# Kernel optimization log

Measured on AMD Instinct MI355X. Metric: run time of the kernel, lower is better.

Reference implementation:

```python
import jax, jax.numpy as jnp
import numpy as np
from jax import lax

WS = 7          # window size
SHIFT = 3       # shift size
HEADS = 16
DIM = 512
NREF = 100
H_IMG = 112
W_IMG = 112
BATCH = 2
HD = DIM // HEADS
SCALE = HD ** (-0.5)
EPS = 1e-5


def _layernorm(x, w, b):
    mu = jnp.mean(x, axis=-1, keepdims=True)
    var = jnp.mean((x - mu) ** 2, axis=-1, keepdims=True)
    return (x - mu) / jnp.sqrt(var + EPS) * w + b


def _rel_pos_index():
    coords = np.stack(np.meshgrid(np.arange(WS), np.arange(WS), indexing='ij'))  # (2,ws,ws)
    cf = coords.reshape(2, -1)
    rel = cf[:, :, None] - cf[:, None, :]
    rel = rel.transpose(1, 2, 0).astype(np.int64)
    rel[..., 0] += WS - 1
    rel[..., 1] += WS - 1
    rel[..., 0] *= 2 * WS - 1
    return rel.sum(-1).reshape(-1)  # (N*N,)

_RPI = _rel_pos_index()


def setup_inputs() -> dict:
    key = jax.random.key(0)
    ks = jax.random.split(key, 16)
    C = DIM
    s = 0.02
    x = jax.random.normal(ks[0], (BATCH, H_IMG * W_IMG, C), jnp.float32)
    x_ref = jax.random.normal(ks[1], (BATCH, NREF, C), jnp.float32)
    # shifted-window attention mask (standard Swin construction)
    img = np.zeros((H_IMG, W_IMG))
    cnt = 0
    for hs in (slice(0, -WS), slice(-WS, -SHIFT), slice(-SHIFT, None)):
        for ws_ in (slice(0, -WS), slice(-WS, -SHIFT), slice(-SHIFT, None)):
            img[hs, ws_] = cnt
            cnt += 1
    mw = img.reshape(H_IMG // WS, WS, W_IMG // WS, WS).transpose(0, 2, 1, 3).reshape(-1, WS * WS)
    am = mw[:, None, :] - mw[:, :, None]
    mask = jnp.asarray(np.where(am != 0, -100.0, 0.0), jnp.float32)  # (nW, N, N)
    return dict(
        x=x, x_ref=x_ref, mask=mask,
        norm1_w=jnp.ones((C,), jnp.float32), norm1_b=jnp.zeros((C,), jnp.float32),
        qkv_w=jax.random.normal(ks[2], (3 * C, C), jnp.float32) * s,
        qkv_b=jnp.zeros((3 * C,), jnp.float32),
        diff_mu=jax.random.normal(ks[3], (1, 1, C), jnp.float32),
        diff_logsigma=jax.random.normal(ks[4], (1, 1, C), jnp.float32) * s,
        rpb_table=jax.random.normal(ks[5], ((2 * WS - 1) ** 2, HEADS), jnp.float32) * s,
        ref_qk_w=jax.random.normal(ks[6], (2 * C, C), jnp.float32) * s,
        ref_qk_b=jnp.zeros((2 * C,), jnp.float32),
        conv_w=jax.random.normal(ks[7], (HEADS, HEADS, 3, 3), jnp.float32) * s,
        conv_b=jnp.zeros((HEADS,), jnp.float32),
        proj_w=jax.random.normal(ks[8], (C, C), jnp.float32) * s,
        proj_b=jnp.zeros((C,), jnp.float32),
        norm2_w=jnp.ones((C,), jnp.float32), norm2_b=jnp.zeros((C,), jnp.float32),
        fc1_w=jax.random.normal(ks[9], (4 * C, C), jnp.float32) * s,
        fc1_b=jnp.zeros((4 * C,), jnp.float32),
        fc2_w=jax.random.normal(ks[10], (C, 4 * C), jnp.float32) * s,
        fc2_b=jnp.zeros((C,), jnp.float32),
        Hh=H_IMG, Ww=W_IMG,
    )


def _window_attention(xw, mask, x_ref, qkv_w, qkv_b, diff_mu, diff_logsigma,
                      rpb_table, ref_qk_w, ref_qk_b, conv_w, conv_b, proj_w, proj_b):
    B_, N, C = xw.shape
    rB = x_ref.shape[0]
    n_win = B_ // rB
    qkv = (xw @ qkv_w.T + qkv_b).reshape(B_, N, 3, HEADS, HD).transpose(2, 0, 3, 1, 4)
    q, k, v = qkv[0], qkv[1], qkv[2]  # (B_, heads, N, hd)
    # reference tokens -> q/v with reparameterized shift/scale
    ref_qk = (x_ref @ ref_qk_w.T + ref_qk_b).reshape(rB, NREF, 2, C).transpose(2, 0, 1, 3)
    ref_q = diff_mu + jnp.exp(diff_logsigma) * ref_qk[0]
    ref_q = ref_q.reshape(rB, NREF, HEADS, HD).transpose(0, 2, 1, 3)
    ref_v = ref_qk[1].reshape(rB, NREF, HEADS, HD).transpose(0, 2, 1, 3)
    ref_k = jnp.repeat(ref_q, n_win, axis=0)  # (B_, heads, nref, hd)
    ref_v = jnp.repeat(ref_v, n_win, axis=0)
    ra = jnp.einsum('bhnd,bhrd->bhnr', q, ref_k)  # (B_, heads, N, nref)
    ra = ra.reshape(rB, n_win, HEADS, N, NREF).transpose(0, 2, 1, 3, 4).reshape(rB, HEADS, n_win * N, NREF)
    # 3 rounds of conv diffusion + layernorm(no affine) + gelu, residual
    for _ in range(3):
        u = lax.conv_general_dilated(ra, conv_w, (1, 1), 'SAME',
                                     dimension_numbers=('NCHW', 'OIHW', 'NCHW'))
        u = u + conv_b[None, :, None, None]
        mu = jnp.mean(u, axis=(-2, -1), keepdims=True)
        var = jnp.mean((u - mu) ** 2, axis=(-2, -1), keepdims=True)
        u = jax.nn.gelu((u - mu) / jnp.sqrt(var + EPS), approximate=False)
        ra = ra + u
    ra = ra.reshape(rB, HEADS, n_win, N, NREF).transpose(0, 2, 1, 3, 4).reshape(B_, HEADS, N, NREF)
    ra = jax.nn.softmax(ra, axis=-1)
    q_new = jnp.einsum('bhnr,bhrd->bhnd', ra, ref_v) * SCALE
    attn = jnp.einsum('bhnd,bhmd->bhnm', q_new, k)
    rpb = rpb_table[_RPI].reshape(N, N, HEADS).transpose(2, 0, 1)  # (heads, N, N)
    attn = attn + rpb[None]
    nW = mask.shape[0]
    attn = attn.reshape(B_ // nW, nW, HEADS, N, N) + mask[None, :, None]
    attn = jax.nn.softmax(attn.reshape(B_, HEADS, N, N), axis=-1)
    out = jnp.einsum('bhnm,bhmd->bhnd', attn, v).transpose(0, 2, 1, 3).reshape(B_, N, C)
    return out @ proj_w.T + proj_b


def reference(x, x_ref, mask, norm1_w, norm1_b, qkv_w, qkv_b, diff_mu, diff_logsigma,
              rpb_table, ref_qk_w, ref_qk_b, conv_w, conv_b, proj_w, proj_b,
              norm2_w, norm2_b, fc1_w, fc1_b, fc2_w, fc2_b, Hh, Ww):
    B, L, C = x.shape
    shortcut = x
    xn = _layernorm(x, norm1_w, norm1_b).reshape(B, Hh, Ww, C)
    # cyclic shift
    sx = jnp.roll(xn, (-SHIFT, -SHIFT), axis=(1, 2))
    # window partition -> (B*nWin, ws*ws, C)
    xw = sx.reshape(B, Hh // WS, WS, Ww // WS, WS, C).transpose(0, 1, 3, 2, 4, 5).reshape(-1, WS * WS, C)
    aw = _window_attention(xw, mask, x_ref, qkv_w, qkv_b, diff_mu, diff_logsigma,
                           rpb_table, ref_qk_w, ref_qk_b, conv_w, conv_b, proj_w, proj_b)
    # window reverse
    sx = aw.reshape(B, Hh // WS, Ww // WS, WS, WS, C).transpose(0, 1, 3, 2, 4, 5).reshape(B, Hh, Ww, C)
    xn = jnp.roll(sx, (SHIFT, SHIFT), axis=(1, 2)).reshape(B, L, C)
    x = shortcut + xn
    h = _layernorm(x, norm2_w, norm2_b)
    h = jax.nn.gelu(h @ fc1_w.T + fc1_b, approximate=False)
    return x + (h @ fc2_w.T + fc2_b)
```

## Files before the change

### kernel.cpp

```cpp
#include <hip/hip_runtime.h>
#include <hip/hip_bf16.h>

typedef __attribute__((ext_vector_type(8))) short short8;
typedef __attribute__((ext_vector_type(8))) unsigned short ushort8;
typedef __attribute__((ext_vector_type(4))) float f32x4;
typedef __attribute__((ext_vector_type(4))) unsigned int u32x4;
typedef __attribute__((ext_vector_type(2))) unsigned int u32x2;

#define DEV __device__ __forceinline__

DEV float gelu_f(float x) { return 0.5f * x * (1.f + erff(x * 0.70710678118654752440f)); }

DEV float bf2f(unsigned short s) {
  unsigned int t = ((unsigned int)s) << 16;
  float f; __builtin_memcpy(&f, &t, 4); return f;
}
DEV unsigned short f2bf(float f) {
  __hip_bfloat16 b = __float2bfloat16(f);
  unsigned short s; __builtin_memcpy(&s, &b, 2); return s;
}

DEV void async_copy16(void* lds, const void* g) {
  __builtin_amdgcn_global_load_lds(
      (const __attribute__((address_space(1))) unsigned int*)g,
      (__attribute__((address_space(3))) unsigned int*)lds, 16, 0, 0);
}

DEV void block_reduce2(float& s, float& s2) {
  __shared__ float red[8];
  int tid = threadIdx.x;
#pragma unroll
  for (int o = 32; o > 0; o >>= 1) { s += __shfl_down(s, o); s2 += __shfl_down(s2, o); }
  if ((tid & 63) == 0) { red[tid >> 6] = s; red[4 + (tid >> 6)] = s2; }
  __syncthreads();
  s  = red[0] + red[1] + red[2] + red[3];
  s2 = red[4] + red[5] + red[6] + red[7];
}

__global__ __launch_bounds__(256) void f2b_kernel(const float* __restrict__ in,
                                                  __hip_bfloat16* __restrict__ o, int n) {
  int i = blockIdx.x * 256 + threadIdx.x;
  if (i < n) o[i] = __float2bfloat16(in[i]);
}

__global__ __launch_bounds__(256) void maskb_kernel(const float* __restrict__ mask,
                                                    unsigned short* __restrict__ maskB) {
  int i = blockIdx.x * 256 + threadIdx.x;
  int m = i % 56, rest = i / 56;
  int n = rest % 49, win = rest / 49;
  unsigned short v = 0;
  if (m < 49) v = f2bf(mask[((size_t)win * 49 + n) * 49 + m]);
  maskB[i] = v;
}

__global__ __launch_bounds__(256) void rpbt_kernel(const float* __restrict__ rpb,
                                                   unsigned short* __restrict__ rpbT) {
  int i = blockIdx.x * 256 + threadIdx.x;
  if (i >= 43904) return;
  int m = i % 56, rest = i / 56;
  int n = rest % 49, h = rest / 49;
  unsigned short v = 0;
  if (m < 49) {
    int rp = (n / 7 - m / 7 + 6) * 13 + (n % 7 - m % 7 + 6);
    v = f2bf(rpb[rp * 16 + h]);
  }
  rpbT[i] = v;
}

__global__ __launch_bounds__(256) void ln1_window_kernel(
    const float* __restrict__ x, const float* __restrict__ w, const float* __restrict__ b,
    __hip_bfloat16* __restrict__ xw) {
  int tid = threadIdx.x;
  int wave = tid >> 6, lane = tid & 63;
  int t = blockIdx.x * 4 + wave;
  int b_ = t / 49, n = t % 49;
  int bb = b_ >> 8, win = b_ & 255;
  int wi = win >> 4, wj = win & 15;
  int ii = n / 7, jj = n % 7;
  int sh = (wi * 7 + ii + 3) % 112;
  int sw = (wj * 7 + jj + 3) % 112;
  const float* row = x + ((size_t)bb * 12544 + sh * 112 + sw) * 512;
  f32x4 v0 = *reinterpret_cast<const f32x4*>(&row[lane * 8]);
  f32x4 v1 = *reinterpret_cast<const f32x4*>(&row[lane * 8 + 4]);
  float s = 0.f, s2 = 0.f;
#pragma unroll
  for (int j = 0; j < 4; j++) {
    s += v0[j] + v1[j];
    s2 += v0[j] * v0[j] + v1[j] * v1[j];
  }
#pragma unroll
  for (int o = 1; o < 64; o <<= 1) { s += __shfl_xor(s, o); s2 += __shfl_xor(s2, o); }
  float mu = s * (1.f / 512.f);
  float rstd = rsqrtf(s2 * (1.f / 512.f) - mu * mu + 1e-5f);
  f32x4 w0 = *reinterpret_cast<const f32x4*>(&w[lane * 8]);
  f32x4 w1 = *reinterpret_cast<const f32x4*>(&w[lane * 8 + 4]);
  f32x4 c0 = *reinterpret_cast<const f32x4*>(&b[lane * 8]);
  f32x4 c1 = *reinterpret_cast<const f32x4*>(&b[lane * 8 + 4]);
  ushort8 o8;
#pragma unroll
  for (int j = 0; j < 4; j++) {
    o8[j]     = f2bf((v0[j] - mu) * rstd * w0[j] + c0[j]);
    o8[4 + j] = f2bf((v1[j] - mu) * rstd * w1[j] + c1[j]);
  }
  *reinterpret_cast<ushort8*>((unsigned short*)xw + (size_t)t * 512 + lane * 8) = o8;
}

template <int EPI>
__global__ __launch_bounds__(256) void gemm_bt(
    const __hip_bfloat16* __restrict__ A, const __hip_bfloat16* __restrict__ B,
    const float* __restrict__ bias, float* __restrict__ outF,
    __hip_bfloat16* __restrict__ outB, int M, int N, int K) {
  __shared__ __align__(16) __hip_bfloat16 As[128 * 64];
  __shared__ __align__(16) __hip_bfloat16 Bs[128 * 64];
  int m0 = blockIdx.x * 128, n0 = blockIdx.y * 128;
  int tid = threadIdx.x;
  int wave = tid >> 6, lane = tid & 63;
  int wm = (wave & 1) * 64, wn = (wave >> 1) * 64;
  int lrow = lane & 15, kq = lane >> 4;
  int srow = lane >> 3, scol = (lane & 7) * 8;
  f32x4 acc[4][4] = {};
  for (int k0 = 0; k0 < K; k0 += 64) {
    int rb = wave * 32;
#pragma unroll
    for (int i = 0; i < 4; i++) {
      int row = rb + i * 8 + srow;
      async_copy16(&As[(rb + i * 8) * 64], &A[(size_t)(m0 + row) * K + k0 + scol]);
      async_copy16(&Bs[(rb + i * 8) * 64], &B[(size_t)(n0 + row) * K + k0 + scol]);
    }
    __syncthreads();
#pragma unroll
    for (int ks = 0; ks < 2; ks++) {
      short8 af[4], bf[4];
#pragma unroll
      for (int t = 0; t < 4; t++) {
        af[t] = *reinterpret_cast<const short8*>(&As[(wm + t * 16 + lrow) * 64 + ks * 32 + kq * 8]);
        bf[t] = *reinterpret_cast<const short8*>(&Bs[(wn + t * 16 + lrow) * 64 + ks * 32 + kq * 8]);
      }
#pragma unroll
      for (int tm = 0; tm < 4; tm++)
#pragma unroll
        for (int tn = 0; tn < 4; tn++)
          acc[tm][tn] = __builtin_amdgcn_mfma_f32_16x16x32_bf16(af[tm], bf[tn], acc[tm][tn], 0, 0, 0);
    }
    __syncthreads();
  }
#pragma unroll
  for (int tm = 0; tm < 4; tm++) {
#pragma unroll
    for (int tn = 0; tn < 4; tn++) {
      int col = n0 + wn + tn * 16 + lrow;
      float bv = bias[col];
#pragma unroll
      for (int r = 0; r < 4; r++) {
        int row = m0 + wm + tm * 16 + kq * 4 + r;
        float v = acc[tm][tn][r] + bv;
        size_t o = (size_t)row * N + col;
        if (EPI == 1) outB[o] = __float2bfloat16(v);
        else if (EPI == 2) outB[o] = __float2bfloat16(gelu_f(v));
        else outF[o] += v;
      }
    }
  }
}

__global__ __launch_bounds__(256) void ref_kernel(
    const float* __restrict__ x_ref, const float* __restrict__ w, const float* __restrict__ bias,
    const float* __restrict__ diff_mu, const float* __restrict__ diff_ls,
    unsigned short* __restrict__ refq, unsigned short* __restrict__ refvT) {
  int blk = blockIdx.x;
  int b = blk / 100, r = blk % 100;
  __shared__ float xs[512];
  int tid = threadIdx.x;
  const float* xr = x_ref + (size_t)(b * 100 + r) * 512;
  xs[tid] = xr[tid];
  xs[tid + 256] = xr[tid + 256];
  __syncthreads();
#pragma unroll
  for (int cc = 0; cc < 4; cc++) {
    int c = cc * 256 + tid;
    const float* wr = w + (size_t)c * 512;
    float s = bias[c];
    for (int k = 0; k < 512; k++) s += xs[k] * wr[k];
    if (c < 512) {
      float v = diff_mu[c] + expf(diff_ls[c]) * s;
      int hh = c >> 5, d = c & 31;
      refq[((size_t)(b * 16 + hh) * 100 + r) * 32 + d] = f2bf(v);
    } else {
      int c2 = c - 512, hh = c2 >> 5, d = c2 & 31;
      refvT[(((size_t)b * 16 + hh) * 32 + d) * 100 + r] = f2bf(s);
    }
  }
}

__global__ __launch_bounds__(256) void ra_kernel(
    const __hip_bfloat16* __restrict__ q, const unsigned short* __restrict__ refq,
    __hip_bfloat16* __restrict__ ra) {
  __shared__ __align__(16) unsigned short q_s[64 * 40];
  __shared__ __align__(16) unsigned short rq_s[112 * 40];
  int blk = blockIdx.x;
  int b_ = blk >> 4, h = blk & 15;
  int rb = b_ >> 8, win = b_ & 255;
  int tid = threadIdx.x;
  int wave = tid >> 6, lane = tid & 63;
  int lrow = lane & 15, kq = lane >> 4;
  u32x4 z4 = {};
  const unsigned short* qb = (const unsigned short*)q + (size_t)b_ * 49 * 512 + h * 32;
  for (int i = tid; i < 196; i += 256) {
    int n = i >> 2, c = i & 3;
    *reinterpret_cast<u32x4*>(&q_s[n * 40 + c * 8]) =
        *reinterpret_cast<const u32x4*>(&qb[n * 512 + c * 8]);
  }
  for (int i = tid; i < 60; i += 256) {
    int n = 49 + (i >> 2), c = i & 3;
    *reinterpret_cast<u32x4*>(&q_s[n * 40 + c * 8]) = z4;
  }
  const unsigned short* rqg = refq + (size_t)(rb * 16 + h) * 3200;
  for (int i = tid; i < 400; i += 256) {
    int r = i >> 2, c = i & 3;
    *reinterpret_cast<u32x4*>(&rq_s[r * 40 + c * 8]) =
        *reinterpret_cast<const u32x4*>(&rqg[r * 32 + c * 8]);
  }
  for (int i = tid; i < 48; i += 256) {
    int r = 100 + (i >> 2), c = i & 3;
    *reinterpret_cast<u32x4*>(&rq_s[r * 40 + c * 8]) = z4;
  }
  __syncthreads();
  short8 a = *reinterpret_cast<const short8*>(&q_s[(wave * 16 + lrow) * 40 + kq * 8]);
  unsigned short* ra_base = (unsigned short*)ra + ((size_t)(rb * 16 + h) * 12544 + win * 49) * 100;
  f32x4 zero = {};
#pragma unroll
  for (int nt = 0; nt < 7; nt++) {
    short8 b = *reinterpret_cast<const short8*>(&rq_s[(nt * 16 + lrow) * 40 + kq * 8]);
    f32x4 c = __builtin_amdgcn_mfma_f32_16x16x32_bf16(a, b, zero, 0, 0, 0);
    int col = nt * 16 + lrow;
#pragma unroll
    for (int r = 0; r < 4; r++) {
      int n = wave * 16 + kq * 4 + r;
      if (n < 49 && col < 100) ra_base[n * 100 + col] = f2bf(c[r]);
    }
  }
}

__global__ __launch_bounds__(256) void conv_kernel(
    const __hip_bfloat16* __restrict__ ra_, const float* __restrict__ cw, const float* __restrict__ cb,
    __hip_bfloat16* __restrict__ u_, float* __restrict__ psum, float* __restrict__ psumsq) {
  __shared__ __align__(16) unsigned short in_s[6 * 103 * 24];
  __shared__ __align__(16) unsigned short w_s[16 * 160];
  __shared__ float sred_s[4][16], sred_s2[4][16];
  const unsigned short* ra = (const unsigned short*)ra_;
  unsigned short* u = (unsigned short*)u_;
  int yt = blockIdx.x, bb = blockIdx.y;
  int y0 = yt * 4;
  int tid = threadIdx.x;
  int wave = tid >> 6, lane = tid & 63;
  int lrow = lane & 15, kq = lane >> 4;
  for (int i = tid; i < 2560; i += 256) {
    int co = i / 160, k = i % 160;
    unsigned short v = 0;
    if (k < 144) {
      int ci = k & 15, p = k >> 4;
      v = f2bf(cw[(co * 16 + ci) * 9 + p]);
    }
    w_s[i] = v;
  }
  for (int i = tid; i < 288; i += 256) {
    int ci = i & 15, rem = i >> 4;
    int yl = rem / 3, xs = rem % 3;
    int xl = (xs == 0) ? 0 : (100 + xs);
    in_s[(yl * 103 + xl) * 24 + ci] = 0;
  }
  if (tid < 192) {
    int unit = tid >> 1, par = tid & 1;
    int ci = unit / 6, yl = unit % 6;
    int gy = y0 - 1 + yl;
    bool rv = (gy >= 0 && gy < 12544);
    const unsigned short* rp = ra + (((size_t)bb * 16 + ci) * 12544 + (rv ? gy : 0)) * 100;
    unsigned short* lp = &in_s[(yl * 103 + 1) * 24 + ci];
#pragma unroll 4
    for (int c = par; c < 25; c += 2) {
      u32x2 d = {0u, 0u};
      if (rv) d = *reinterpret_cast<const u32x2*>(&rp[c * 4]);
      lp[(c * 4 + 0) * 24] = (unsigned short)(d[0] & 0xffff);
      lp[(c * 4 + 1) * 24] = (unsigned short)(d[0] >> 16);
      lp[(c * 4 + 2) * 24] = (unsigned short)(d[1] & 0xffff);
      lp[(c * 4 + 3) * 24] = (unsigned short)(d[1] >> 16);
    }
  }
  __syncthreads();

  short8 afr[5];
#pragma unroll
  for (int c = 0; c < 5; c++)
    afr[c] = *reinterpret_cast<const short8*>(&w_s[lrow * 160 + c * 32 + kq * 8]);
  int kqh = kq >> 1, ci0 = (kq & 1) * 8;
  int kyA[5], kxA[5];
#pragma unroll
  for (int c = 0; c < 5; c++) {
    int p = c * 2 + kqh; if (p > 8) p = 0;
    kyA[c] = p / 3; kxA[c] = p % 3;
  }
  float bias_r[4];
#pragma unroll
  for (int r = 0; r < 4; r++) bias_r[r] = cb[kq * 4 + r];
  float s_r[4] = {0.f, 0.f, 0.f, 0.f}, s2_r[4] = {0.f, 0.f, 0.f, 0.f};

  int yl = wave;
  int gy = y0 + yl;
#pragma unroll
  for (int xg = 0; xg < 7; xg++) {
    int px = xg * 16 + lrow;
    int pxc = px < 100 ? px : 99;
    f32x4 acc = {};
#pragma unroll
    for (int c = 0; c < 5; c++) {
      short8 bfrag = *reinterpret_cast<const short8*>(
          &in_s[((yl + kyA[c]) * 103 + pxc + kxA[c]) * 24 + ci0]);
      acc = __builtin_amdgcn_mfma_f32_16x16x32_bf16(afr[c], bfrag, acc, 0, 0, 0);
    }
    bool valid = px < 100;
#pragma unroll
    for (int r = 0; r < 4; r++) {
      float v = acc[r] + bias_r[r];
      if (valid) {
        u[(((size_t)bb * 16 + kq * 4 + r) * 12544 + gy) * 100 + px] = f2bf(v);
        s_r[r] += v; s2_r[r] += v * v;
      }
    }
  }
#pragma unroll
  for (int o = 1; o < 16; o <<= 1)
#pragma unroll
    for (int r = 0; r < 4; r++) { s_r[r] += __shfl_xor(s_r[r], o); s2_r[r] += __shfl_xor(s2_r[r], o); }
  if (lrow == 0)
#pragma unroll
    for (int r = 0; r < 4; r++) { sred_s[wave][kq * 4 + r] = s_r[r]; sred_s2[wave][kq * 4 + r] = s2_r[r]; }
  __syncthreads();
  if (tid < 16) {
    float s  = sred_s[0][tid] + sred_s[1][tid] + sred_s[2][tid] + sred_s[3][tid];
    float s2 = sred_s2[0][tid] + sred_s2[1][tid] + sred_s2[2][tid] + sred_s2[3][tid];
    size_t pi = ((size_t)bb * 3136 + yt) * 16 + tid;
    psum[pi] = s; psumsq[pi] = s2;
  }
}

__global__ __launch_bounds__(256) void conv_stats_kernel(
    const float* __restrict__ psum, const float* __restrict__ psumsq, float* __restrict__ stats) {
  int g = blockIdx.x;
  int bb = g >> 4, co = g & 15;
  int tid = threadIdx.x;
  float s = 0.f, s2 = 0.f;
  for (int t = tid; t < 3136; t += 256) {
    size_t pi = ((size_t)bb * 3136 + t) * 16 + co;
    s += psum[pi];
    s2 += psumsq[pi];
  }
  block_reduce2(s, s2);
  if (tid == 0) {
    const float inv = 1.f / 1254400.f;
    float mu = s * inv;
    float var = s2 * inv - mu * mu;
    stats[g * 2] = mu;
    stats[g * 2 + 1] = rsqrtf(var + 1e-5f);
  }
}

__global__ __launch_bounds__(256) void conv_apply_kernel(
    __hip_bfloat16* __restrict__ ra, const __hip_bfloat16* __restrict__ u,
    const float* __restrict__ stats) {
  const int total8 = 5017600;
  int stride = gridDim.x * 256;
  for (int i = blockIdx.x * 256 + threadIdx.x; i < total8; i += stride) {
    int g = i / 156800;
    float mu = stats[g * 2], rstd = stats[g * 2 + 1];
    ushort8 uu = reinterpret_cast<const ushort8*>(u)[i];
    ushort8 rr = reinterpret_cast<const ushort8*>(ra)[i];
    ushort8 oo;
#pragma unroll
    for (int j = 0; j < 8; j++) {
      float rv = bf2f(rr[j]) + gelu_f((bf2f(uu[j]) - mu) * rstd);
      oo[j] = f2bf(rv);
    }
    reinterpret_cast<ushort8*>(ra)[i] = oo;
  }
}

template <int FUSE>
__global__ __launch_bounds__(256) void attn_kernel(
    const __hip_bfloat16* __restrict__ ra_, const __hip_bfloat16* __restrict__ u_,
    const float* __restrict__ stats, const unsigned short* __restrict__ refvT,
    const __hip_bfloat16* __restrict__ kv_, const unsigned short* __restrict__ rpbT,
    const unsigned short* __restrict__ maskB, __hip_bfloat16* __restrict__ att_) {
  __shared__ __align__(16) char smem[27136];
  unsigned short* P1  = (unsigned short*)smem;
  unsigned short* rvT = (unsigned short*)(smem + 13312);
  unsigned short* qn  = (unsigned short*)(smem + 22016);
  unsigned short* P2  = (unsigned short*)smem;
  unsigned short* vT  = (unsigned short*)(smem + 9216);
  unsigned short* kb  = (unsigned short*)(smem + 13824);

#define LSUM(n) (*reinterpret_cast<float*>(&qn[(n) * 40 + 32]))

  int blk = blockIdx.x;
  int b_ = blk >> 4, h = blk & 15;
  int rb = b_ >> 8, win = b_ & 255;
  int tid = threadIdx.x;
  int wave = tid >> 6, lane = tid & 63;
  int lrow = lane & 15, kq = lane >> 4;
  const unsigned short* ra = (const unsigned short*)ra_;
  const unsigned short* ug = (const unsigned short*)u_;
  const unsigned short* kv = (const unsigned short*)kv_;
  unsigned short* att = (unsigned short*)att_;
  u32x2 zz = {};

  if (tid < 64) LSUM(tid) = 1.0f;
  float mu = 0.f, rstd = 0.f;
  if (FUSE) { mu = stats[(rb * 16 + h) * 2]; rstd = stats[(rb * 16 + h) * 2 + 1]; }

  const size_t tile_off = ((size_t)(rb * 16 + h) * 12544 + win * 49) * 100;
  const unsigned short* rab = ra + tile_off;
  const unsigned short* uab = ug + tile_off;
  for (int i = tid; i < 1225; i += 256) {
    int n = i / 25, c = i % 25;
    u32x2 rv = *reinterpret_cast<const u32x2*>(&rab[n * 100 + c * 4]);
    if (FUSE) {
      u32x2 uv = *reinterpret_cast<const u32x2*>(&uab[n * 100 + c * 4]);
      unsigned short rr4[4] = {(unsigned short)(rv[0] & 0xffff), (unsigned short)(rv[0] >> 16),
                               (unsigned short)(rv[1] & 0xffff), (unsigned short)(rv[1] >> 16)};
      unsigned short uu4[4] = {(unsigned short)(uv[0] & 0xffff), (unsigned short)(uv[0] >> 16),
                               (unsigned short)(uv[1] & 0xffff), (unsigned short)(uv[1] >> 16)};
      unsigned short o4[4];
#pragma unroll
      for (int j = 0; j < 4; j++)
        o4[j] = f2bf(bf2f(rr4[j]) + gelu_f((bf2f(uu4[j]) - mu) * rstd));
      u32x2 w;
      w[0] = (unsigned int)o4[0] | ((unsigned int)o4[1] << 16);
      w[1] = (unsigned int)o4[2] | ((unsigned int)o4[3] << 16);
      *reinterpret_cast<u32x2*>(&P1[n * 136 + c * 4]) = w;
    } else {
      *reinterpret_cast<u32x2*>(&P1[n * 136 + c * 4]) = rv;
    }
  }
  for (int i = tid; i < 343; i += 256) {
    int n = i / 7, c = i % 7;
    *reinterpret_cast<u32x2*>(&P1[n * 136 + 100 + c * 4]) = zz;
  }
  const unsigned short* rvtg = refvT + (size_t)(rb * 16 + h) * 3200;
  for (int i = tid; i < 800; i += 256) {
    int d = i / 25, c = i % 25;
    *reinterpret_cast<u32x2*>(&rvT[d * 136 + c * 4]) =
        *reinterpret_cast<const u32x2*>(&rvtg[d * 100 + c * 4]);
  }
  for (int i = tid; i < 224; i += 256) {
    int d = i / 7, c = i % 7;
    *reinterpret_cast<u32x2*>(&rvT[d * 136 + 100 + c * 4]) = zz;
  }
  __syncthreads();

  if (tid < 196) {
    int n = tid >> 2, q = tid & 3;
    unsigned short* row = P1 + n * 136 + q * 25;
    float e[25];
#pragma unroll
    for (int r = 0; r < 25; r++) e[r] = bf2f(row[r]);
    float mx = -1e30f;
#pragma unroll
    for (int r = 0; r < 25; r++) mx = fmaxf(mx, e[r]);
    mx = fmaxf(mx, __shfl_xor(mx, 1));
    mx = fmaxf(mx, __shfl_xor(mx, 2));
    float sm = 0.f;
#pragma unroll
    for (int r = 0; r < 25; r++) { e[r] = __expf(e[r] - mx); sm += e[r]; }
    sm += __shfl_xor(sm, 1);
    sm += __shfl_xor(sm, 2);
#pragma unroll
    for (int r = 0; r < 25; r++) row[r] = f2bf(e[r]);
    if (q == 0) LSUM(n) = sm;
  }
  __syncthreads();

  f32x4 acc1[2] = {};
#pragma unroll
  for (int ks = 0; ks < 4; ks++) {
    short8 a = *reinterpret_cast<const short8*>(&P1[(wave * 16 + lrow) * 136 + ks * 32 + kq * 8]);
#pragma unroll
    for (int dt = 0; dt < 2; dt++) {
      short8 b = *reinterpret_cast<const short8*>(&rvT[(dt * 16 + lrow) * 136 + ks * 32 + kq * 8]);
      acc1[dt] = __builtin_amdgcn_mfma_f32_16x16x32_bf16(a, b, acc1[dt], 0, 0, 0);
    }
  }
  float invl[4];
#pragma unroll
  for (int r = 0; r < 4; r++)
    invl[r] = 0.17677669529663688f / LSUM(wave * 16 + kq * 4 + r);
#pragma unroll
  for (int dt = 0; dt < 2; dt++)
#pragma unroll
    for (int r = 0; r < 4; r++) {
      int n = wave * 16 + kq * 4 + r;
      qn[n * 40 + dt * 16 + lrow] = f2bf(acc1[dt][r] * invl[r]);
    }
  __syncthreads();

  const unsigned short* kvb = kv + (size_t)b_ * 49 * 1024;
  for (int i = tid; i < 196; i += 256) {
    int m = i >> 2, c = i & 3;
    *reinterpret_cast<u32x4*>(&kb[m * 40 + c * 8]) =
        *reinterpret_cast<const u32x4*>(&kvb[m * 1024 + h * 32 + c * 8]);
  }
  for (int i = tid; i < 196; i += 256) {
    int m = i >> 2, dg = (i & 3) * 8;
    ushort8 vv = *reinterpret_cast<const ushort8*>(&kvb[m * 1024 + 512 + h * 32 + dg]);
#pragma unroll
    for (int j = 0; j < 8; j++) vT[(dg + j) * 72 + m] = vv[j];
  }
  for (int i = tid; i < 480; i += 256) vT[(i / 15) * 72 + 49 + i % 15] = 0;
  __syncthreads();

  const unsigned short* bt = maskB + (size_t)win * 2744;
  const unsigned short* rt = rpbT + (size_t)h * 2744;
  short8 aq = *reinterpret_cast<const short8*>(&qn[(wave * 16 + lrow) * 40 + kq * 8]);
  f32x4 zero = {};
  float val[4][4];
#pragma unroll
  for (int mt = 0; mt < 4; mt++) {
    short8 bk = *reinterpret_cast<const short8*>(&kb[(mt * 16 + lrow) * 40 + kq * 8]);
    f32x4 lg = __builtin_amdgcn_mfma_f32_16x16x32_bf16(aq, bk, zero, 0, 0, 0);
    int m = mt * 16 + lrow;
#pragma unroll
    for (int r = 0; r < 4; r++) {
      int n = wave * 16 + kq * 4 + r;
      float v;
      if (m < 49 && n < 49)
        v = lg[r] + bf2f(rt[n * 56 + m]) + bf2f(bt[n * 56 + m]);
      else v = -1e30f;
      val[mt][r] = v;
    }
  }
#pragma unroll
  for (int r = 0; r < 4; r++) {
    float mx = -1e30f;
#pragma unroll
    for (int mt = 0; mt < 4; mt++) mx = fmaxf(mx, val[mt][r]);
    mx = fmaxf(mx, __shfl_xor(mx, 1)); mx = fmaxf(mx, __shfl_xor(mx, 2));
    mx = fmaxf(mx, __shfl_xor(mx, 4)); mx = fmaxf(mx, __shfl_xor(mx, 8));
    float sm = 0.f, e[4];
#pragma unroll
    for (int mt = 0; mt < 4; mt++) { e[mt] = __expf(val[mt][r] - mx); sm += e[mt]; }
    sm += __shfl_xor(sm, 1); sm += __shfl_xor(sm, 2);
    sm += __shfl_xor(sm, 4); sm += __shfl_xor(sm, 8);
    float inv = 1.f / sm;
    int n = wave * 16 + kq * 4 + r;
#pragma unroll
    for (int mt = 0; mt < 4; mt++) P2[n * 72 + mt * 16 + lrow] = f2bf(e[mt] * inv);
  }
  __syncthreads();

  f32x4 acc2[2] = {};
#pragma unroll
  for (int ks = 0; ks < 2; ks++) {
    short8 ap = *reinterpret_cast<const short8*>(&P2[(wave * 16 + lrow) * 72 + ks * 32 + kq * 8]);
#pragma unroll
    for (int dt = 0; dt < 2; dt++) {
      short8 bv = *reinterpret_cast<const short8*>(&vT[(dt * 16 + lrow) * 72 + ks * 32 + kq * 8]);
      acc2[dt] = __builtin_amdgcn_mfma_f32_16x16x32_bf16(ap, bv, acc2[dt], 0, 0, 0);
    }
  }
  unsigned short* ab = att + (size_t)b_ * 49 * 512 + h * 32;
#pragma unroll
  for (int dt = 0; dt < 2; dt++)
#pragma unroll
    for (int r = 0; r < 4; r++) {
      int n = wave * 16 + kq * 4 + r;
      if (n < 49) ab[n * 512 + dt * 16 + lrow] = f2bf(acc2[dt][r]);
    }
#undef LSUM
}

__global__ __launch_bounds__(256) void resid_ln2_kernel(
    const float* __restrict__ x, const __hip_bfloat16* __restrict__ proj_out,
    const float* __restrict__ w2, const float* __restrict__ b2,
    float* __restrict__ out, __hip_bfloat16* __restrict__ hout) {
  int tid = threadIdx.x;
  int wave = tid >> 6, lane = tid & 63;
  int blk = blockIdx.x * 4 + wave;
  int bb = blk / 12544, l = blk % 12544;
  int hh = l / 112, ww = l % 112;
  int hs = (hh + 109) % 112, wsx = (ww + 109) % 112;
  int t = (bb * 256 + (hs / 7) * 16 + (wsx / 7)) * 49 + (hs % 7) * 7 + (wsx % 7);
  const float* xr = x + (size_t)blk * 512 + lane * 8;
  const unsigned short* pr = (const unsigned short*)proj_out + (size_t)t * 512 + lane * 8;
  f32x4 x0 = *reinterpret_cast<const f32x4*>(xr);
  f32x4 x1 = *reinterpret_cast<const f32x4*>(xr + 4);
  ushort8 p8 = *reinterpret_cast<const ushort8*>(pr);
  float v[8];
#pragma unroll
  for (int j = 0; j < 4; j++) {
    v[j]     = x0[j] + bf2f(p8[j]);
    v[4 + j] = x1[j] + bf2f(p8[4 + j]);
  }
  float s = 0.f, s2 = 0.f;
#pragma unroll
  for (int j = 0; j < 8; j++) { s += v[j]; s2 += v[j] * v[j]; }
  float* orow = out + (size_t)blk * 512 + lane * 8;
  f32x4 o0, o1;
#pragma unroll
  for (int j = 0; j < 4; j++) { o0[j] = v[j]; o1[j] = v[4 + j]; }
  *reinterpret_cast<f32x4*>(orow) = o0;
  *reinterpret_cast<f32x4*>(orow + 4) = o1;
#pragma unroll
  for (int o = 1; o < 64; o <<= 1) { s += __shfl_xor(s, o); s2 += __shfl_xor(s2, o); }
  float mu = s * (1.f / 512.f);
  float rstd = rsqrtf(s2 * (1.f / 512.f) - mu * mu + 1e-5f);
  f32x4 w0 = *reinterpret_cast<const f32x4*>(&w2[lane * 8]);
  f32x4 w1 = *reinterpret_cast<const f32x4*>(&w2[lane * 8 + 4]);
  f32x4 c0 = *reinterpret_cast<const f32x4*>(&b2[lane * 8]);
  f32x4 c1 = *reinterpret_cast<const f32x4*>(&b2[lane * 8 + 4]);
  ushort8 h8;
#pragma unroll
  for (int j = 0; j < 4; j++) {
    h8[j]     = f2bf((v[j] - mu) * rstd * w0[j] + c0[j]);
    h8[4 + j] = f2bf((v[4 + j] - mu) * rstd * w1[j] + c1[j]);
  }
  *reinterpret_cast<ushort8*>((unsigned short*)hout + (size_t)blk * 512 + lane * 8) = h8;
}

extern "C" void kernel_launch(void* const* d_in, const int* in_sizes, int n_in,
                              void* d_out, int out_size, void* d_ws, size_t ws_size,
                              hipStream_t stream) {
  const float* x       = (const float*)d_in[0];
  const float* x_ref   = (const float*)d_in[1];
  const float* mask    = (const float*)d_in[2];
  const float* n1w     = (const float*)d_in[3];
  const float* n1b     = (const float*)d_in[4];
  const float* qkv_w   = (const float*)d_in[5];
  const float* qkv_b   = (const float*)d_in[6];
  const float* diff_mu = (const float*)d_in[7];
  const float* diff_ls = (const float*)d_in[8];
  const float* rpb     = (const float*)d_in[9];
  const float* ref_w   = (const float*)d_in[10];
  const float* ref_b   = (const float*)d_in[11];
  const float* conv_w  = (const float*)d_in[12];
  const float* conv_b  = (const float*)d_in[13];
  const float* proj_w  = (const float*)d_in[14];
  const float* proj_b  = (const float*)d_in[15];
  const float* n2w     = (const float*)d_in[16];
  const float* n2b     = (const float*)d_in[17];
  const float* fc1_w   = (const float*)d_in[18];
  const float* fc1_b   = (const float*)d_in[19];
  const float* fc2_w   = (const float*)d_in[20];
  const float* fc2_b   = (const float*)d_in[21];
  float* out = (float*)d_out;

  char* ws = (char*)d_ws;
  size_t off = 0;
  auto alloc = [&](size_t bytes) -> char* {
    char* p = ws + off;
    off += (bytes + 255) & ~(size_t)255;
    return p;
  };
  __hip_bfloat16* wq_bf = (__hip_bfloat16*)alloc(1536ULL * 512 * 2);
  __hip_bfloat16* wp_bf = (__hip_bfloat16*)alloc(512ULL * 512 * 2);
  __hip_bfloat16* w1_bf = (__hip_bfloat16*)alloc(2048ULL * 512 * 2);
  __hip_bfloat16* w2_bf = (__hip_bfloat16*)alloc(512ULL * 2048 * 2);
  unsigned short* refq  = (unsigned short*)alloc(2ULL * 16 * 100 * 32 * 2);
  unsigned short* refvT = (unsigned short*)alloc(2ULL * 16 * 32 * 100 * 2);
  unsigned short* maskB = (unsigned short*)alloc(256ULL * 49 * 56 * 2);
  unsigned short* rpbT  = (unsigned short*)alloc(16ULL * 49 * 56 * 2);
  float* psum  = (float*)alloc(2ULL * 3136 * 16 * 4);
  float* psumq = (float*)alloc(2ULL * 3136 * 16 * 4);
  float* stats = (float*)alloc(64 * 4);
  char* regX  = alloc(25088ULL * 512 * 2);
  char* regQ  = alloc(25088ULL * 512 * 2);
  char* regRA = alloc(2ULL * 16 * 12544 * 100 * 2);
  char* regU  = alloc(2ULL * 16 * 12544 * 100 * 2);

  __hip_bfloat16* xw_bf   = (__hip_bfloat16*)regX;
  __hip_bfloat16* att_bf  = (__hip_bfloat16*)regX;
  __hip_bfloat16* q_bf    = (__hip_bfloat16*)regQ;
  __hip_bfloat16* h_bf    = (__hip_bfloat16*)regQ;
  __hip_bfloat16* ra      = (__hip_bfloat16*)regRA;
  __hip_bfloat16* hg      = (__hip_bfloat16*)regRA;
  __hip_bfloat16* u       = (__hip_bfloat16*)regU;
  __hip_bfloat16* proj_bf = (__hip_bfloat16*)(regU + 51380224);

  const size_t kv_bytes = 25088ULL * 1024 * 2;
  bool fused = (ws_size >= off + kv_bytes);
  __hip_bfloat16* kv_bf = fused ? (__hip_bfloat16*)alloc(kv_bytes)
                                : (__hip_bfloat16*)regU;

  f2b_kernel<<<3072, 256, 0, stream>>>(qkv_w, wq_bf, 786432);
  f2b_kernel<<<1024, 256, 0, stream>>>(proj_w, wp_bf, 262144);
  f2b_kernel<<<4096, 256, 0, stream>>>(fc1_w, w1_bf, 1048576);
  f2b_kernel<<<4096, 256, 0, stream>>>(fc2_w, w2_bf, 1048576);
  maskb_kernel<<<2744, 256, 0, stream>>>(mask, maskB);
  rpbt_kernel<<<172, 256, 0, stream>>>(rpb, rpbT);
  ln1_window_kernel<<<6272, 256, 0, stream>>>(x, n1w, n1b, xw_bf);
  gemm_bt<1><<<dim3(196, 4), 256, 0, stream>>>(xw_bf, wq_bf, qkv_b, nullptr, q_bf,
                                               25088, 512, 512);
  ref_kernel<<<200, 256, 0, stream>>>(x_ref, ref_w, ref_b, diff_mu, diff_ls, refq, refvT);
  ra_kernel<<<8192, 256, 0, stream>>>(q_bf, refq, ra);
  for (int rd = 0; rd < 3; rd++) {
    conv_kernel<<<dim3(3136, 2), 256, 0, stream>>>(ra, conv_w, conv_b, u, psum, psumq);
    conv_stats_kernel<<<32, 256, 0, stream>>>(psum, psumq, stats);
    if (rd < 2 || !fused)
      conv_apply_kernel<<<4096, 256, 0, stream>>>(ra, u, stats);
  }
  gemm_bt<1><<<dim3(196, 8), 256, 0, stream>>>(xw_bf, wq_bf + 512 * 512, qkv_b + 512,
                                               nullptr, kv_bf, 25088, 1024, 512);
  if (fused)
    attn_kernel<1><<<8192, 256, 0, stream>>>(ra, u, stats, refvT, kv_bf, rpbT, maskB, att_bf);
  else
    attn_kernel<0><<<8192, 256, 0, stream>>>(ra, u, stats, refvT, kv_bf, rpbT, maskB, att_bf);
  gemm_bt<1><<<dim3(196, 4), 256, 0, stream>>>(att_bf, wp_bf, proj_b, nullptr, proj_bf,
                                               25088, 512, 512);
  resid_ln2_kernel<<<6272, 256, 0, stream>>>(x, proj_bf, n2w, n2b, out, h_bf);
  for (int ch = 0; ch < 2; ch++) {
    const __hip_bfloat16* hA = h_bf + (size_t)ch * 12544 * 512;
    gemm_bt<2><<<dim3(98, 16), 256, 0, stream>>>(hA, w1_bf, fc1_b, nullptr, hg,
                                                 12544, 2048, 512);
    gemm_bt<3><<<dim3(98, 4), 256, 0, stream>>>(hg, w2_bf, fc2_b,
                                                out + (size_t)ch * 12544 * 512, nullptr,
                                                12544, 512, 2048);
  }
}
```

Baseline: 1.160 ms.

## Read refvT and K MFMA operands directly from global, shrink attention LDS

The reference-value transpose buffer is padded to a stride of 128 with zeroed tail columns, so the attention kernel can load MFMA B operands for the P1·refV product straight from global memory. The K operand for the logits MFMA is also loaded from global, with out-of-range rows clamped. This removes two LDS staging loops and their space, cutting shared memory from about 27 KB to 19 KB and adding a min-blocks launch bound of 8 to raise occupancy. In exchange, MFMA operands come from scattered global/L2 reads instead of LDS.

```diff
diff --git a/kernel.cpp b/kernel.cpp
--- a/kernel.cpp
+++ b/kernel.cpp
@@ -187,7 +187,15 @@
       refq[((size_t)(b * 16 + hh) * 100 + r) * 32 + d] = f2bf(v);
     } else {
       int c2 = c - 512, hh = c2 >> 5, d = c2 & 31;
-      refvT[(((size_t)b * 16 + hh) * 32 + d) * 100 + r] = f2bf(s);
+      refvT[(((size_t)b * 16 + hh) * 32 + d) * 128 + r] = f2bf(s);
+    }
+  }
+  if (r < 28) {
+#pragma unroll
+    for (int j = 0; j < 2; j++) {
+      int idx = j * 256 + tid;
+      int hh = idx >> 5, d = idx & 31;
+      refvT[(((size_t)b * 16 + hh) * 32 + d) * 128 + 100 + r] = 0;
     }
   }
 }
@@ -385,18 +393,16 @@
 }
 
 template <int FUSE>
-__global__ __launch_bounds__(256) void attn_kernel(
+__global__ __launch_bounds__(256, 8) void attn_kernel(
     const __hip_bfloat16* __restrict__ ra_, const __hip_bfloat16* __restrict__ u_,
     const float* __restrict__ stats, const unsigned short* __restrict__ refvT,
     const __hip_bfloat16* __restrict__ kv_, const unsigned short* __restrict__ rpbT,
     const unsigned short* __restrict__ maskB, __hip_bfloat16* __restrict__ att_) {
-  __shared__ __align__(16) char smem[27136];
-  unsigned short* P1  = (unsigned short*)smem;
-  unsigned short* rvT = (unsigned short*)(smem + 13312);
-  unsigned short* qn  = (unsigned short*)(smem + 22016);
-  unsigned short* P2  = (unsigned short*)smem;
-  unsigned short* vT  = (unsigned short*)(smem + 9216);
-  unsigned short* kb  = (unsigned short*)(smem + 13824);
+  __shared__ __align__(16) char smem[18944];
+  unsigned short* P1 = (unsigned short*)smem;
+  unsigned short* P2 = (unsigned short*)smem;
+  unsigned short* vT = (unsigned short*)(smem + 9216);
+  unsigned short* qn = (unsigned short*)(smem + 13824);
 
 #define LSUM(n) (*reinterpret_cast<float*>(&qn[(n) * 40 + 32]))
 
@@ -444,16 +450,6 @@
     int n = i / 7, c = i % 7;
     *reinterpret_cast<u32x2*>(&P1[n * 136 + 100 + c * 4]) = zz;
   }
-  const unsigned short* rvtg = refvT + (size_t)(rb * 16 + h) * 3200;
-  for (int i = tid; i < 800; i += 256) {
-    int d = i / 25, c = i % 25;
-    *reinterpret_cast<u32x2*>(&rvT[d * 136 + c * 4]) =
-        *reinterpret_cast<const u32x2*>(&rvtg[d * 100 + c * 4]);
-  }
-  for (int i = tid; i < 224; i += 256) {
-    int d = i / 7, c = i % 7;
-    *reinterpret_cast<u32x2*>(&rvT[d * 136 + 100 + c * 4]) = zz;
-  }
   __syncthreads();
 
   if (tid < 196) {
@@ -478,13 +474,14 @@
   }
   __syncthreads();
 
+  const unsigned short* rvtg = refvT + (size_t)(rb * 16 + h) * 4096;
   f32x4 acc1[2] = {};
 #pragma unroll
   for (int ks = 0; ks < 4; ks++) {
     short8 a = *reinterpret_cast<const short8*>(&P1[(wave * 16 + lrow) * 136 + ks * 32 + kq * 8]);
 #pragma unroll
     for (int dt = 0; dt < 2; dt++) {
-      short8 b = *reinterpret_cast<const short8*>(&rvT[(dt * 16 + lrow) * 136 + ks * 32 + kq * 8]);
+      short8 b = *reinterpret_cast<const short8*>(&rvtg[(dt * 16 + lrow) * 128 + ks * 32 + kq * 8]);
       acc1[dt] = __builtin_amdgcn_mfma_f32_16x16x32_bf16(a, b, acc1[dt], 0, 0, 0);
     }
   }
@@ -502,11 +499,6 @@
   __syncthreads();
 
   const unsigned short* kvb = kv + (size_t)b_ * 49 * 1024;
-  for (int i = tid; i < 196; i += 256) {
-    int m = i >> 2, c = i & 3;
-    *reinterpret_cast<u32x4*>(&kb[m * 40 + c * 8]) =
-        *reinterpret_cast<const u32x4*>(&kvb[m * 1024 + h * 32 + c * 8]);
-  }
   for (int i = tid; i < 196; i += 256) {
     int m = i >> 2, dg = (i & 3) * 8;
     ushort8 vv = *reinterpret_cast<const ushort8*>(&kvb[m * 1024 + 512 + h * 32 + dg]);
@@ -523,9 +515,11 @@
   float val[4][4];
 #pragma unroll
   for (int mt = 0; mt < 4; mt++) {
-    short8 bk = *reinterpret_cast<const short8*>(&kb[(mt * 16 + lrow) * 40 + kq * 8]);
+    int mrow = mt * 16 + lrow;
+    int mc = mrow < 49 ? mrow : 48;
+    short8 bk = *reinterpret_cast<const short8*>(&kvb[mc * 1024 + h * 32 + kq * 8]);
     f32x4 lg = __builtin_amdgcn_mfma_f32_16x16x32_bf16(aq, bk, zero, 0, 0, 0);
-    int m = mt * 16 + lrow;
+    int m = mrow;
 #pragma unroll
     for (int r = 0; r < 4; r++) {
       int n = wave * 16 + kq * 4 + r;
@@ -663,7 +657,7 @@
   __hip_bfloat16* w1_bf = (__hip_bfloat16*)alloc(2048ULL * 512 * 2);
   __hip_bfloat16* w2_bf = (__hip_bfloat16*)alloc(512ULL * 2048 * 2);
   unsigned short* refq  = (unsigned short*)alloc(2ULL * 16 * 100 * 32 * 2);
-  unsigned short* refvT = (unsigned short*)alloc(2ULL * 16 * 32 * 100 * 2);
+  unsigned short* refvT = (unsigned short*)alloc(2ULL * 16 * 32 * 128 * 2);
   unsigned short* maskB = (unsigned short*)alloc(256ULL * 49 * 56 * 2);
   unsigned short* rpbT  = (unsigned short*)alloc(16ULL * 49 * 56 * 2);
   float* psum  = (float*)alloc(2ULL * 3136 * 16 * 4);
```

New measurement: 1.157 ms. Within noise of the previous version (-0.3%).
